# Optimization experiments

Measured on AMD Instinct MI355X. Metric: run time of the kernel, lower is better.

## Reference

```python
import jax, jax.numpy as jnp
import numpy as np

D_MODEL = 1024
H = 16
D_FF = 2048
EPS = 1e-5


def _ln(x, g, b):
    m = jnp.mean(x, axis=-1, keepdims=True)
    v = jnp.mean((x - m) ** 2, axis=-1, keepdims=True)
    return (x - m) * jax.lax.rsqrt(v + EPS) * g + b


def setup_inputs() -> dict:
    key = jax.random.key(0)
    ks = jax.random.split(key, 16)
    d, dff = D_MODEL, D_FF
    s = 1.0 / np.sqrt(d)
    inp = {
        "x": jax.random.normal(ks[0], (2, 2048, d), jnp.float32),
        "Wq": jax.random.normal(ks[1], (d, d), jnp.float32) * s,
        "bq": jax.random.normal(ks[2], (d,), jnp.float32) * 0.01,
        "Wk": jax.random.normal(ks[3], (d, d), jnp.float32) * s,
        "bk": jax.random.normal(ks[4], (d,), jnp.float32) * 0.01,
        "Wv": jax.random.normal(ks[5], (d, d), jnp.float32) * s,
        "bv": jax.random.normal(ks[6], (d,), jnp.float32) * 0.01,
        "Wo": jax.random.normal(ks[7], (d, d), jnp.float32) * s,
        "bo": jax.random.normal(ks[8], (d,), jnp.float32) * 0.01,
        "ln1_g": 1.0 + 0.1 * jax.random.normal(ks[9], (d,), jnp.float32),
        "ln1_b": 0.01 * jax.random.normal(ks[10], (d,), jnp.float32),
        "ln2_g": 1.0 + 0.1 * jax.random.normal(ks[11], (d,), jnp.float32),
        "ln2_b": 0.01 * jax.random.normal(ks[12], (d,), jnp.float32),
        "W1": jax.random.normal(ks[13], (d, dff), jnp.float32) * s,
        "b1": 0.01 * jax.random.normal(ks[14], (dff,), jnp.float32),
        "W2": jax.random.normal(ks[15], (dff, d), jnp.float32) * (1.0 / np.sqrt(dff)),
        "b2": jnp.zeros((d,), jnp.float32),
    }
    return inp


def reference(x, Wq, bq, Wk, bk, Wv, bv, Wo, bo, ln1_g, ln1_b, ln2_g, ln2_b, W1, b1, W2, b2):
    b, s, d = x.shape
    dk = d // H

    # --- sublayer 1: pre-LN self-attention with residual (dropout = eval/identity) ---
    y = _ln(x, ln1_g, ln1_b)
    q = (y @ Wq + bq).reshape(b, s, H, dk).transpose(0, 2, 1, 3)  # (b,h,s,dk)
    k = (y @ Wk + bk).reshape(b, s, H, dk).transpose(0, 2, 1, 3)
    v = (y @ Wv + bv).reshape(b, s, H, dk).transpose(0, 2, 1, 3)
    scores = jnp.einsum("bhqd,bhkd->bhqk", q, k) / jnp.sqrt(jnp.float32(dk))
    attn = jax.nn.softmax(scores, axis=-1)
    o = jnp.einsum("bhqk,bhkd->bhqd", attn, v)  # (b,h,s,dk)
    # faithful to original bug: transpose last two dims then flat reshape
    o = jnp.swapaxes(o, -1, -2).reshape(b, s, d)  # (b,h,dk,s) -> (b,s,d)
    x = x + (o @ Wo + bo)

    # --- sublayer 2: pre-LN FFN with residual ---
    y2 = _ln(x, ln2_g, ln2_b)
    f = jax.nn.relu(y2 @ W1 + b1) @ W2 + b2
    return x + f
```

## Files before the change

### kernel.cpp

```cpp
#include <hip/hip_runtime.h>
#include <hip/hip_bf16.h>

#define D_MODEL 1024
#define NHEAD 16
#define DK 64
#define DFF 2048
#define SEQ 2048
#define NBATCH 2
#define NTOK (NBATCH*SEQ)

typedef __attribute__((ext_vector_type(8))) short bf16x8;
typedef __attribute__((ext_vector_type(4))) float f32x4;
typedef __attribute__((ext_vector_type(16))) float f32x16;
typedef __attribute__((ext_vector_type(4))) short s16x4;

#if __has_builtin(__builtin_amdgcn_exp2f)
#define EXP2(x) __builtin_amdgcn_exp2f(x)
#else
#define EXP2(x) exp2f(x)
#endif

__device__ __forceinline__ short f2bf(float f) {
    union { float f; unsigned u; } v; v.f = f;
    unsigned r = v.u + 0x7FFFu + ((v.u >> 16) & 1u);
    return (short)(r >> 16);
}

__device__ __forceinline__ void gld16(void* lds, const void* g) {
    __builtin_amdgcn_global_load_lds(
        (const __attribute__((address_space(1))) void*)g,
        (__attribute__((address_space(3))) void*)lds, 16, 0, 0);
}

struct TP6 { const float* src[6]; short* dst[6]; int K[6], N[6], nx[6]; };
__global__ __launch_bounds__(256) void k_prolog(TP6 tp, const float* __restrict__ x,
                                                const float* __restrict__ g,
                                                const float* __restrict__ bta,
                                                short* __restrict__ y)
{
    __shared__ float t[32][33];
    int id = blockIdx.x;
    if (id >= 8192) {
        int row = (id - 8192) * 4 + (threadIdx.x >> 6);
        int lane = threadIdx.x & 63;
        const float* xr = x + (size_t)row * D_MODEL;
        float4 v[4];
        float s = 0.f, s2 = 0.f;
#pragma unroll
        for (int c = 0; c < 4; ++c) {
            v[c] = *(const float4*)(xr + c * 256 + lane * 4);
            s  += v[c].x + v[c].y + v[c].z + v[c].w;
            s2 += v[c].x * v[c].x + v[c].y * v[c].y + v[c].z * v[c].z + v[c].w * v[c].w;
        }
#pragma unroll
        for (int off = 1; off < 64; off <<= 1) {
            s  += __shfl_xor(s, off, 64);
            s2 += __shfl_xor(s2, off, 64);
        }
        float mean = s * (1.f / 1024.f);
        float var  = s2 * (1.f / 1024.f) - mean * mean;
        float rs = rsqrtf(var + 1e-5f);
        short* yr = y + (size_t)row * D_MODEL;
#pragma unroll
        for (int c = 0; c < 4; ++c) {
            int idx = c * 256 + lane * 4;
            float4 gg = *(const float4*)(g + idx);
            float4 bb = *(const float4*)(bta + idx);
            s16x4 o;
            o.x = f2bf((v[c].x - mean) * rs * gg.x + bb.x);
            o.y = f2bf((v[c].y - mean) * rs * gg.y + bb.y);
            o.z = f2bf((v[c].z - mean) * rs * gg.z + bb.z);
            o.w = f2bf((v[c].w - mean) * rs * gg.w + bb.w);
            *(s16x4*)(yr + idx) = o;
        }
        return;
    }
    int seg, tt;
    if (id < 4096)      { seg = id >> 10; tt = id & 1023; }
    else if (id < 6144) { seg = 4; tt = id - 4096; }
    else                { seg = 5; tt = id - 6144; }
    const float* W = tp.src[seg];
    short* WT = tp.dst[seg];
    int K = tp.K[seg], N = tp.N[seg], nx = tp.nx[seg];
    int bx = tt % nx, by = tt / nx;
    int tid = threadIdx.x;
    int n0 = bx * 32, k0 = by * 32;
#pragma unroll
    for (int p = 0; p < 4; ++p) {
        int idx = p * 256 + tid, r = idx >> 5, c = idx & 31;
        t[r][c] = W[(size_t)(k0 + r) * N + (n0 + c)];
    }
    __syncthreads();
#pragma unroll
    for (int p = 0; p < 4; ++p) {
        int idx = p * 256 + tid, r = idx >> 5, c = idx & 31;
        WT[(size_t)(n0 + r) * K + (k0 + c)] = f2bf(t[c][r]);
    }
}

__global__ __launch_bounds__(256) void k_layernorm(const float* __restrict__ x,
                                                   const float* __restrict__ g,
                                                   const float* __restrict__ bta,
                                                   short* __restrict__ y)
{
    int row = blockIdx.x * 4 + (threadIdx.x >> 6);
    int lane = threadIdx.x & 63;
    const float* xr = x + (size_t)row * D_MODEL;
    float4 v[4];
    float s = 0.f, s2 = 0.f;
#pragma unroll
    for (int c = 0; c < 4; ++c) {
        v[c] = *(const float4*)(xr + c * 256 + lane * 4);
        s  += v[c].x + v[c].y + v[c].z + v[c].w;
        s2 += v[c].x * v[c].x + v[c].y * v[c].y + v[c].z * v[c].z + v[c].w * v[c].w;
    }
#pragma unroll
    for (int off = 1; off < 64; off <<= 1) {
        s  += __shfl_xor(s, off, 64);
        s2 += __shfl_xor(s2, off, 64);
    }
    float mean = s * (1.f / 1024.f);
    float var  = s2 * (1.f / 1024.f) - mean * mean;
    float rs = rsqrtf(var + 1e-5f);
    short* yr = y + (size_t)row * D_MODEL;
#pragma unroll
    for (int c = 0; c < 4; ++c) {
        int idx = c * 256 + lane * 4;
        float4 gg = *(const float4*)(g + idx);
        float4 bb = *(const float4*)(bta + idx);
        s16x4 o;
        o.x = f2bf((v[c].x - mean) * rs * gg.x + bb.x);
        o.y = f2bf((v[c].y - mean) * rs * gg.y + bb.y);
        o.z = f2bf((v[c].z - mean) * rs * gg.z + bb.z);
        o.w = f2bf((v[c].w - mean) * rs * gg.w + bb.w);
        *(s16x4*)(yr + idx) = o;
    }
}

template<int EPI, int BN, int THREADS>
__global__ __launch_bounds__(THREADS, (THREADS == 512) ? 8 : 4) void k_gemm(
    const short* __restrict__ A, const short* __restrict__ BT, int N, int K,
    const float* __restrict__ bias, const float* __restrict__ bias2, const float* __restrict__ bias3,
    const float* __restrict__ resid, float* __restrict__ outF,
    short* __restrict__ outB, short* __restrict__ outQ, short* __restrict__ outK, short* __restrict__ outV)
{
    constexpr int CW = (THREADS == 512) ? 4 : 2;
    __shared__ __align__(16) short sA[3][128 * 32];
    __shared__ __align__(16) short sB[3][BN * 32];
    int tid = threadIdx.x;
    int lane = tid & 63, wid = tid >> 6;
    int wr = wid / CW, wc = wid % CW;
    int l31 = lane & 31, hi = lane >> 5;

    int gx = gridDim.x;
    int nwg = gx * gridDim.y;
    int orig = blockIdx.x + blockIdx.y * gx;
    int wg = (orig & 7) * (nwg >> 3) + (orig >> 3);
    int bx = wg % gx, by = wg / gx;

    const short* Ab = A + (size_t)by * 128 * K;
    const short* Bb = BT + (size_t)bx * BN * K;

    auto src = [&](const short* base, int cc) {
        int r = cc >> 2, s = cc & 3;
        return (const char*)(base + (size_t)r * K) + ((s ^ ((r >> 1) & 3)) << 4);
    };
    const char *pA0 = src(Ab, tid), *pA1 = nullptr, *pB0;
    if constexpr (THREADS == 512) {
        pB0 = src(Bb, tid);
    } else {
        pA1 = src(Ab, 256 + tid);
        pB0 = src(Bb, tid & (BN * 4 - 1));
    }

    auto stage = [&](int buf) {
        if constexpr (THREADS == 512) {
            gld16(&sA[buf][tid * 8], pA0);  pA0 += 64;
            gld16(&sB[buf][tid * 8], pB0);  pB0 += 64;
        } else {
            gld16(&sA[buf][tid * 8], pA0);          pA0 += 64;
            gld16(&sA[buf][(256 + tid) * 8], pA1);  pA1 += 64;
            gld16(&sB[buf][(tid & (BN * 4 - 1)) * 8], pB0);  pB0 += 64;
        }
    };

    f32x16 acc0 = {0,0,0,0,0,0,0,0,0,0,0,0,0,0,0,0};
    f32x16 acc1 = {0,0,0,0,0,0,0,0,0,0,0,0,0,0,0,0};

    const int NT = K / 32;
    stage(0);
    stage(1);
    int cur = 0;
    for (int t = 0; t < NT; ++t) {
        if (t + 2 < NT) {
            int nb3 = cur + 2; if (nb3 >= 3) nb3 -= 3;
            stage(nb3);
            if constexpr (THREADS == 512) asm volatile("s_waitcnt vmcnt(4)" ::: "memory");
            else                          asm volatile("s_waitcnt vmcnt(6)" ::: "memory");
        } else if (t + 1 < NT) {
            if constexpr (THREADS == 512) asm volatile("s_waitcnt vmcnt(2)" ::: "memory");
            else                          asm volatile("s_waitcnt vmcnt(3)" ::: "memory");
        } else {
            asm volatile("s_waitcnt vmcnt(0)" ::: "memory");
        }
        __builtin_amdgcn_s_barrier();
        int rb = wc * 32 + l31;
        int swb = (rb >> 1) & 3;
        bf16x8 b0 = *(const bf16x8*)((const char*)sB[cur] + rb * 64 + ((hi ^ swb) << 4));
        bf16x8 b1 = *(const bf16x8*)((const char*)sB[cur] + rb * 64 + (((2 + hi) ^ swb) << 4));
        {
            int ra = wr * 64 + l31;
            int swa = (ra >> 1) & 3;
            bf16x8 a0 = *(const bf16x8*)((const char*)sA[cur] + ra * 64 + ((hi ^ swa) << 4));
            acc0 = __builtin_amdgcn_mfma_f32_32x32x16_bf16(a0, b0, acc0, 0, 0, 0);
            bf16x8 a1 = *(const bf16x8*)((const char*)sA[cur] + ra * 64 + (((2 + hi) ^ swa) << 4));
            acc0 = __builtin_amdgcn_mfma_f32_32x32x16_bf16(a1, b1, acc0, 0, 0, 0);
        }
        {
            int ra = wr * 64 + 32 + l31;
            int swa = (ra >> 1) & 3;
            bf16x8 a0 = *(const bf16x8*)((const char*)sA[cur] + ra * 64 + ((hi ^ swa) << 4));
            acc1 = __builtin_amdgcn_mfma_f32_32x32x16_bf16(a0, b0, acc1, 0, 0, 0);
            bf16x8 a1 = *(const bf16x8*)((const char*)sA[cur] + ra * 64 + (((2 + hi) ^ swa) << 4));
            acc1 = __builtin_amdgcn_mfma_f32_32x32x16_bf16(a1, b1, acc1, 0, 0, 0);
        }
        __builtin_amdgcn_s_barrier();
        ++cur; if (cur >= 3) cur = 0;
    }

    int n = bx * BN + wc * 32 + l31;
    int mb = by * 128 + wr * 64 + 4 * hi;
    if constexpr (EPI == 0) {
        int seg = n >> 10, nn = n & 1023;
        int h = nn >> 6, dd = nn & 63;
        int bb = (by * 128) >> 11;
        if (seg == 0) {
            float bs = bias[nn];
            short* p = outQ + (size_t)(bb * NHEAD + h) * SEQ * DK + dd;
#pragma unroll
            for (int i = 0; i < 2; ++i)
#pragma unroll
                for (int reg = 0; reg < 16; ++reg) {
                    int ss = (mb + i * 32 + (reg & 3) + 8 * (reg >> 2)) & 2047;
                    float v = (i == 0) ? acc0[reg] : acc1[reg];
                    p[(size_t)ss * DK] = f2bf((v + bs) * 0.18033688011112042f);
                }
        } else if (seg == 1) {
            float bs = bias2[nn];
            short* p = outK + (size_t)(bb * NHEAD + h) * SEQ * DK + dd;
#pragma unroll
            for (int i = 0; i < 2; ++i)
#pragma unroll
                for (int reg = 0; reg < 16; ++reg) {
                    int ss = (mb + i * 32 + (reg & 3) + 8 * (reg >> 2)) & 2047;
                    float v = (i == 0) ? acc0[reg] : acc1[reg];
                    p[(size_t)ss * DK] = f2bf(v + bs);
                }
        } else {
            float bs = bias3[nn];
            short* p = outV + ((size_t)(bb * NHEAD + h) * DK + dd) * SEQ;
#pragma unroll
            for (int i = 0; i < 2; ++i)
#pragma unroll
                for (int reg = 0; reg < 16; ++reg) {
                    int ss = (mb + i * 32 + (reg & 3) + 8 * (reg >> 2)) & 2047;
                    float v = (i == 0) ? acc0[reg] : acc1[reg];
                    p[ss] = f2bf(v + bs);
                }
        }
    } else if constexpr (EPI == 1 || EPI == 3) {
        float bs = bias[n];
#pragma unroll
        for (int i = 0; i < 2; ++i)
#pragma unroll
            for (int reg = 0; reg < 16; ++reg) {
                int m = mb + i * 32 + (reg & 3) + 8 * (reg >> 2);
                float v = (i == 0) ? acc0[reg] : acc1[reg];
                size_t idx = (size_t)m * N + n;
                outF[idx] = v + bs + resid[idx];
            }
    } else {
        float bs = bias[n];
#pragma unroll
        for (int i = 0; i < 2; ++i)
#pragma unroll
            for (int reg = 0; reg < 16; ++reg) {
                int m = mb + i * 32 + (reg & 3) + 8 * (reg >> 2);
                float v = (i == 0) ? acc0[reg] : acc1[reg];
                float r2 = v + bs;
                outB[(size_t)m * N + n] = f2bf(r2 > 0.f ? r2 : 0.f);
            }
    }
}

__global__ __launch_bounds__(256) void k_attn(const short* __restrict__ Q, const short* __restrict__ Kk,
                                              const short* __restrict__ Vt, short* __restrict__ Operm)
{
    __shared__ __align__(16) short sMem[2][2][64 * 64];
    int tid = threadIdx.x, lane = tid & 63;
    int wid = tid >> 6;
    int qg = wid >> 1, ks = wid & 1;
    int l31 = lane & 31, hi = lane >> 5;

    int orig = blockIdx.x + blockIdx.y * 32;
    int lg = (orig & 7) * 128 + (orig >> 3);
    int bh = lg >> 5, qt = lg & 31;
    int b = bh >> 4, h = bh & 15;
    int q0 = qt * 64 + qg * 32;
    const short* Qp = Q + (size_t)bh * SEQ * DK;
    const short* Kp = Kk + (size_t)bh * SEQ * DK;
    const short* Vp = Vt + (size_t)bh * DK * SEQ;

    bf16x8 qf[4];
#pragma unroll
    for (int kb = 0; kb < 4; ++kb)
        qf[kb] = *(const bf16x8*)(Qp + (size_t)(q0 + l31) * DK + kb * 16 + hi * 8);

    int c0 = tid, c1 = 256 + tid;
    int r0 = c0 >> 3, r1 = c1 >> 3;
    const char* pK0 = (const char*)(Kp + (size_t)r0 * DK) + (((c0 & 7) ^ (r0 & 7)) << 4);
    const char* pK1 = (const char*)(Kp + (size_t)r1 * DK) + (((c1 & 7) ^ (r1 & 7)) << 4);
    const char* pV0 = (const char*)(Vp + (size_t)r0 * SEQ) + (((c0 & 7) ^ (r0 & 7)) << 4);
    const char* pV1 = (const char*)(Vp + (size_t)r1 * SEQ) + (((c1 & 7) ^ (r1 & 7)) << 4);

    auto stage = [&](int buf) {
        gld16(&sMem[buf][0][c0 * 8], pK0);  pK0 += 8192;
        gld16(&sMem[buf][0][c1 * 8], pK1);  pK1 += 8192;
        gld16(&sMem[buf][1][c0 * 8], pV0);  pV0 += 128;
        gld16(&sMem[buf][1][c1 * 8], pV1);  pV1 += 128;
    };

    f32x16 Oa0 = {0,0,0,0,0,0,0,0,0,0,0,0,0,0,0,0};
    f32x16 Oa1 = {0,0,0,0,0,0,0,0,0,0,0,0,0,0,0,0};
    float lsum = 0.f;

    stage(0);
    const int NT = SEQ / 64;
    int krow = ks * 32 + l31;
    int sw = (l31 & 7) << 4;
    for (int t = 0; t < NT; ++t) {
        int cur = t & 1;
        if (t + 1 < NT) {
            stage(cur ^ 1);
            asm volatile("s_waitcnt vmcnt(4)" ::: "memory");
        } else {
            asm volatile("s_waitcnt vmcnt(0)" ::: "memory");
        }
        __builtin_amdgcn_s_barrier();
        const char* sKc = (const char*)sMem[cur][0];
        const char* sVc = (const char*)sMem[cur][1];

        f32x16 sc = {0,0,0,0,0,0,0,0,0,0,0,0,0,0,0,0};
        __builtin_amdgcn_s_setprio(1);
#pragma unroll
        for (int kb = 0; kb < 4; ++kb) {
            int cb = (kb * 32 + hi * 16) ^ sw;
            bf16x8 kf = *(const bf16x8*)(sKc + krow * 128 + cb);
            sc = __builtin_amdgcn_mfma_f32_32x32x16_bf16(kf, qf[kb], sc, 0, 0, 0);
        }
        __builtin_amdgcn_s_setprio(0);

        unsigned W[4][2];
#pragma unroll
        for (int tt = 0; tt < 4; ++tt) {
            float pa_ = EXP2(sc[4*tt+0]), pb_ = EXP2(sc[4*tt+1]);
            float pc_ = EXP2(sc[4*tt+2]), pd_ = EXP2(sc[4*tt+3]);
            lsum += (pa_ + pb_) + (pc_ + pd_);
            asm("v_cvt_pk_bf16_f32 %0, %1, %2" : "=v"(W[tt][0]) : "v"(pa_), "v"(pb_));
            asm("v_cvt_pk_bf16_f32 %0, %1, %2" : "=v"(W[tt][1]) : "v"(pc_), "v"(pd_));
        }

        auto pv_step = [&](unsigned a0, unsigned a1, unsigned b0v, unsigned b1v, int kslice) {
            asm("v_permlane32_swap_b32 %0, %1" : "+v"(a0), "+v"(b0v));
            asm("v_permlane32_swap_b32 %0, %1" : "+v"(a1), "+v"(b1v));
            union { unsigned u[4]; bf16x8 v; } pa;
            pa.u[0] = a0; pa.u[1] = a1; pa.u[2] = b0v; pa.u[3] = b1v;
            int cb = (kslice * 32 + hi * 16) ^ sw;
            bf16x8 vf0 = *(const bf16x8*)(sVc + l31 * 128 + cb);
            bf16x8 vf1 = *(const bf16x8*)(sVc + (32 + l31) * 128 + cb);
            Oa0 = __builtin_amdgcn_mfma_f32_32x32x16_bf16(pa.v, vf0, Oa0, 0, 0, 0);
            Oa1 = __builtin_amdgcn_mfma_f32_32x32x16_bf16(pa.v, vf1, Oa1, 0, 0, 0);
        };
        __builtin_amdgcn_s_setprio(1);
        pv_step(W[0][0], W[0][1], W[1][0], W[1][1], ks * 2 + 0);
        pv_step(W[2][0], W[2][1], W[3][0], W[3][1], ks * 2 + 1);
        __builtin_amdgcn_s_setprio(0);
        __builtin_amdgcn_s_barrier();
    }

    lsum += __shfl_xor(lsum, 32, 64);

    float* mrg = (float*)sMem;
    if (ks == 1) {
        float* m0 = mrg + (qg * 64 + lane) * 33;
#pragma unroll
        for (int i = 0; i < 16; ++i) m0[i] = Oa0[i];
#pragma unroll
        for (int i = 0; i < 16; ++i) m0[16 + i] = Oa1[i];
        m0[32] = lsum;
    }
    __syncthreads();
    if (ks == 0) {
        const float* m0 = mrg + (qg * 64 + lane) * 33;
#pragma unroll
        for (int i = 0; i < 16; ++i) Oa0[i] += m0[i];
#pragma unroll
        for (int i = 0; i < 16; ++i) Oa1[i] += m0[16 + i];
        lsum += m0[32];

        float rlv[16];
#pragma unroll
        for (int tt = 0; tt < 4; ++tt)
#pragma unroll
            for (int rr = 0; rr < 4; ++rr) {
                float ts = __shfl(lsum, 4 * hi + 8 * tt + rr, 64);
                rlv[4 * tt + rr] = 1.f / ts;
            }

        int qcol = (q0 & 1023) + 4 * hi;
        int qhi = q0 >> 10;
#pragma unroll
        for (int db = 0; db < 2; ++db) {
            const f32x16& O = db ? Oa1 : Oa0;
            int dd = db * 32 + l31;
            size_t rowoff = ((size_t)b * SEQ + h * 128 + 2 * dd + qhi) * D_MODEL + qcol;
#pragma unroll
            for (int tt = 0; tt < 4; ++tt) {
                s16x4 o;
                o.x = f2bf(O[4*tt+0] * rlv[4*tt+0]);
                o.y = f2bf(O[4*tt+1] * rlv[4*tt+1]);
                o.z = f2bf(O[4*tt+2] * rlv[4*tt+2]);
                o.w = f2bf(O[4*tt+3] * rlv[4*tt+3]);
                *(s16x4*)(Operm + rowoff + 8 * tt) = o;
            }
        }
    }
}

extern "C" void kernel_launch(void* const* d_in, const int* in_sizes, int n_in,
                              void* d_out, int out_size, void* d_ws, size_t ws_size,
                              hipStream_t stream)
{
    const float* x   = (const float*)d_in[0];
    const float* Wq  = (const float*)d_in[1];
    const float* bq  = (const float*)d_in[2];
    const float* Wk  = (const float*)d_in[3];
    const float* bk  = (const float*)d_in[4];
    const float* Wv  = (const float*)d_in[5];
    const float* bv  = (const float*)d_in[6];
    const float* Wo  = (const float*)d_in[7];
    const float* bo  = (const float*)d_in[8];
    const float* g1  = (const float*)d_in[9];
    const float* b1l = (const float*)d_in[10];
    const float* g2  = (const float*)d_in[11];
    const float* b2l = (const float*)d_in[12];
    const float* W1  = (const float*)d_in[13];
    const float* b1  = (const float*)d_in[14];
    const float* W2  = (const float*)d_in[15];
    const float* b2  = (const float*)d_in[16];
    float* out = (float*)d_out;

    char* ws = (char*)d_ws;
    size_t off = 0;
    auto alloc = [&](size_t bytes) {
        char* p = ws + off;
        off += (bytes + 255) & ~(size_t)255;
        return p;
    };
    short* WqkvT = (short*)alloc((size_t)3072 * 1024 * 2);
    short* WoT   = (short*)alloc((size_t)1024 * 1024 * 2);
    short* W1T   = (short*)alloc((size_t)2048 * 1024 * 2);
    short* W2T   = (short*)alloc((size_t)1024 * 2048 * 2);
    short* Y     = (short*)alloc((size_t)NTOK * 1024 * 2);
    short* Qb    = (short*)alloc((size_t)NTOK * 1024 * 2);
    short* Kb    = (short*)alloc((size_t)NTOK * 1024 * 2);
    short* Vtb   = (short*)alloc((size_t)NTOK * 1024 * 2);
    short* Operm = (short*)alloc((size_t)NTOK * 1024 * 2);
    float* X1    = (float*)alloc((size_t)NTOK * 1024 * 4);
    short* F1    = (short*)alloc((size_t)NTOK * 2048 * 2);

    TP6 tp;
    tp.src[0] = Wq; tp.dst[0] = WqkvT;                tp.K[0] = 1024; tp.N[0] = 1024; tp.nx[0] = 32;
    tp.src[1] = Wk; tp.dst[1] = WqkvT + 1024 * 1024;  tp.K[1] = 1024; tp.N[1] = 1024; tp.nx[1] = 32;
    tp.src[2] = Wv; tp.dst[2] = WqkvT + 2048 * 1024;  tp.K[2] = 1024; tp.N[2] = 1024; tp.nx[2] = 32;
    tp.src[3] = Wo; tp.dst[3] = WoT;                  tp.K[3] = 1024; tp.N[3] = 1024; tp.nx[3] = 32;
    tp.src[4] = W1; tp.dst[4] = W1T;                  tp.K[4] = 1024; tp.N[4] = 2048; tp.nx[4] = 64;
    tp.src[5] = W2; tp.dst[5] = W2T;                  tp.K[5] = 2048; tp.N[5] = 1024; tp.nx[5] = 32;
    k_prolog<<<8192 + 1024, 256, 0, stream>>>(tp, x, g1, b1l, Y);

    k_gemm<0,128,512><<<dim3(24, 32), 512, 0, stream>>>(Y, WqkvT, 3072, 1024,
        bq, bk, bv, nullptr, nullptr, nullptr, Qb, Kb, Vtb);

    k_attn<<<dim3(32, 32), 256, 0, stream>>>(Qb, Kb, Vtb, Operm);

    k_gemm<1,64,256><<<dim3(16, 32), 256, 0, stream>>>(Operm, WoT, 1024, 1024,
        bo, nullptr, nullptr, x, X1, nullptr, nullptr, nullptr, nullptr);

    k_layernorm<<<NTOK / 4, 256, 0, stream>>>(X1, g2, b2l, Y);

    k_gemm<2,128,512><<<dim3(16, 32), 512, 0, stream>>>(Y, W1T, 2048, 1024,
        b1, nullptr, nullptr, nullptr, nullptr, F1, nullptr, nullptr, nullptr);

    k_gemm<3,64,256><<<dim3(16, 32), 256, 0, stream>>>(F1, W2T, 1024, 2048,
        b2, nullptr, nullptr, X1, out, nullptr, nullptr, nullptr, nullptr);
}
```

Baseline: 195.2 us.

## Use 256x128 block tiles with 2x2 MFMA per wave for QKV and FFN1 GEMMs

Adds a new GEMM kernel for the QKV projection and the first FFN layer. It uses 256x128 tiles with 8 waves, each computing a 64x64 sub-tile through a 2x2 grid of 32x32 MFMAs, and drops from triple to double LDS buffering. This gives more reuse of each loaded fragment and fewer global loads per FLOP. In exchange the grid is halved, so fewer workgroups fill the CUs, registers per wave go up, and there is less prefetch depth to hide latency.

```diff
diff --git a/kernel.cpp b/kernel.cpp
--- a/kernel.cpp
+++ b/kernel.cpp
@@ -137,19 +137,17 @@
     }
 }
 
-template<int EPI, int BN, int THREADS>
-__global__ __launch_bounds__(THREADS, (THREADS == 512) ? 8 : 4) void k_gemm(
+template<int EPI>
+__global__ __launch_bounds__(512, 4) void k_gemm_big(
     const short* __restrict__ A, const short* __restrict__ BT, int N, int K,
     const float* __restrict__ bias, const float* __restrict__ bias2, const float* __restrict__ bias3,
-    const float* __restrict__ resid, float* __restrict__ outF,
     short* __restrict__ outB, short* __restrict__ outQ, short* __restrict__ outK, short* __restrict__ outV)
 {
-    constexpr int CW = (THREADS == 512) ? 4 : 2;
-    __shared__ __align__(16) short sA[3][128 * 32];
-    __shared__ __align__(16) short sB[3][BN * 32];
+    __shared__ __align__(16) short sA[2][256 * 32];
+    __shared__ __align__(16) short sB[2][128 * 32];
     int tid = threadIdx.x;
     int lane = tid & 63, wid = tid >> 6;
-    int wr = wid / CW, wc = wid % CW;
+    int wr = wid >> 1, wc = wid & 1;
     int l31 = lane & 31, hi = lane >> 5;
 
     int gx = gridDim.x;
@@ -158,30 +156,152 @@
     int wg = (orig & 7) * (nwg >> 3) + (orig >> 3);
     int bx = wg % gx, by = wg / gx;
 
-    const short* Ab = A + (size_t)by * 128 * K;
-    const short* Bb = BT + (size_t)bx * BN * K;
+    const short* Ab = A + (size_t)by * 256 * K;
+    const short* Bb = BT + (size_t)bx * 128 * K;
 
     auto src = [&](const short* base, int cc) {
         int r = cc >> 2, s = cc & 3;
         return (const char*)(base + (size_t)r * K) + ((s ^ ((r >> 1) & 3)) << 4);
     };
-    const char *pA0 = src(Ab, tid), *pA1 = nullptr, *pB0;
-    if constexpr (THREADS == 512) {
-        pB0 = src(Bb, tid);
+    const char* pA0 = src(Ab, tid);
+    const char* pA1 = src(Ab, 512 + tid);
+    const char* pB0 = src(Bb, tid);
+
+    auto stage = [&](int buf) {
+        gld16(&sA[buf][tid * 8], pA0);          pA0 += 64;
+        gld16(&sA[buf][(512 + tid) * 8], pA1);  pA1 += 64;
+        gld16(&sB[buf][tid * 8], pB0);          pB0 += 64;
+    };
+
+    f32x16 acc[2][2];
+#pragma unroll
+    for (int i = 0; i < 2; ++i)
+#pragma unroll
+        for (int j = 0; j < 2; ++j)
+            acc[i][j] = (f32x16){0,0,0,0,0,0,0,0,0,0,0,0,0,0,0,0};
+
+    const int NT = K / 32;
+    stage(0);
+    for (int t = 0; t < NT; ++t) {
+        int cur = t & 1;
+        if (t + 1 < NT) {
+            stage(cur ^ 1);
+            asm volatile("s_waitcnt vmcnt(3)" ::: "memory");
+        } else {
+            asm volatile("s_waitcnt vmcnt(0)" ::: "memory");
+        }
+        __builtin_amdgcn_s_barrier();
+        const char* sAc = (const char*)sA[cur];
+        const char* sBc = (const char*)sB[cur];
+#pragma unroll
+        for (int ksub = 0; ksub < 2; ++ksub) {
+            int sl = ksub * 2 + hi;
+            int rb0 = wc * 64 + l31, rb1 = rb0 + 32;
+            bf16x8 b0 = *(const bf16x8*)(sBc + rb0 * 64 + ((sl ^ ((rb0 >> 1) & 3)) << 4));
+            bf16x8 b1 = *(const bf16x8*)(sBc + rb1 * 64 + ((sl ^ ((rb1 >> 1) & 3)) << 4));
+            int ra0 = wr * 64 + l31, ra1 = ra0 + 32;
+            bf16x8 a0 = *(const bf16x8*)(sAc + ra0 * 64 + ((sl ^ ((ra0 >> 1) & 3)) << 4));
+            bf16x8 a1 = *(const bf16x8*)(sAc + ra1 * 64 + ((sl ^ ((ra1 >> 1) & 3)) << 4));
+            acc[0][0] = __builtin_amdgcn_mfma_f32_32x32x16_bf16(a0, b0, acc[0][0], 0, 0, 0);
+            acc[0][1] = __builtin_amdgcn_mfma_f32_32x32x16_bf16(a0, b1, acc[0][1], 0, 0, 0);
+            acc[1][0] = __builtin_amdgcn_mfma_f32_32x32x16_bf16(a1, b0, acc[1][0], 0, 0, 0);
+            acc[1][1] = __builtin_amdgcn_mfma_f32_32x32x16_bf16(a1, b1, acc[1][1], 0, 0, 0);
+        }
+        __builtin_amdgcn_s_barrier();
+    }
+
+    int nb = bx * 128 + wc * 64 + l31;
+    int mb = by * 256 + wr * 64 + 4 * hi;
+    if constexpr (EPI == 0) {
+        int seg = nb >> 10;
+        int bb = (by * 256) >> 11;
+#pragma unroll
+        for (int j = 0; j < 2; ++j) {
+            int nn = (nb + j * 32) & 1023;
+            int h = nn >> 6, dd = nn & 63;
+            if (seg == 0) {
+                float bs = bias[nn];
+                short* p = outQ + (size_t)(bb * NHEAD + h) * SEQ * DK + dd;
+#pragma unroll
+                for (int i = 0; i < 2; ++i)
+#pragma unroll
+                    for (int reg = 0; reg < 16; ++reg) {
+                        int ss = (mb + i * 32 + (reg & 3) + 8 * (reg >> 2)) & 2047;
+                        p[(size_t)ss * DK] = f2bf((acc[i][j][reg] + bs) * 0.18033688011112042f);
+                    }
+            } else if (seg == 1) {
+                float bs = bias2[nn];
+                short* p = outK + (size_t)(bb * NHEAD + h) * SEQ * DK + dd;
+#pragma unroll
+                for (int i = 0; i < 2; ++i)
+#pragma unroll
+                    for (int reg = 0; reg < 16; ++reg) {
+                        int ss = (mb + i * 32 + (reg & 3) + 8 * (reg >> 2)) & 2047;
+                        p[(size_t)ss * DK] = f2bf(acc[i][j][reg] + bs);
+                    }
+            } else {
+                float bs = bias3[nn];
+                short* p = outV + ((size_t)(bb * NHEAD + h) * DK + dd) * SEQ;
+#pragma unroll
+                for (int i = 0; i < 2; ++i)
+#pragma unroll
+                    for (int reg = 0; reg < 16; ++reg) {
+                        int ss = (mb + i * 32 + (reg & 3) + 8 * (reg >> 2)) & 2047;
+                        p[ss] = f2bf(acc[i][j][reg] + bs);
+                    }
+            }
+        }
     } else {
-        pA1 = src(Ab, 256 + tid);
-        pB0 = src(Bb, tid & (BN * 4 - 1));
-    }
+#pragma unroll
+        for (int j = 0; j < 2; ++j) {
+            int n = nb + j * 32;
+            float bs = bias[n];
+#pragma unroll
+            for (int i = 0; i < 2; ++i)
+#pragma unroll
+                for (int reg = 0; reg < 16; ++reg) {
+                    int m = mb + i * 32 + (reg & 3) + 8 * (reg >> 2);
+                    float r2 = acc[i][j][reg] + bs;
+                    outB[(size_t)m * N + n] = f2bf(r2 > 0.f ? r2 : 0.f);
+                }
+        }
+    }
+}
+
+template<int EPI>
+__global__ __launch_bounds__(256, 4) void k_gemm(
+    const short* __restrict__ A, const short* __restrict__ BT, int N, int K,
+    const float* __restrict__ bias, const float* __restrict__ resid, float* __restrict__ outF)
+{
+    constexpr int BN = 64;
+    __shared__ __align__(16) short sA[3][128 * 32];
+    __shared__ __align__(16) short sB[3][BN * 32];
+    int tid = threadIdx.x;
+    int lane = tid & 63, wid = tid >> 6;
+    int wr = wid >> 1, wc = wid & 1;
+    int l31 = lane & 31, hi = lane >> 5;
+
+    int gx = gridDim.x;
+    int nwg = gx * gridDim.y;
+    int orig = blockIdx.x + blockIdx.y * gx;
+    int wg = (orig & 7) * (nwg >> 3) + (orig >> 3);
+    int bx = wg % gx, by = wg / gx;
+
+    const short* Ab = A + (size_t)by * 128 * K;
+    const short* Bb = BT + (size_t)bx * BN * K;
+
+    auto src = [&](const short* base, int cc) {
+        int r = cc >> 2, s = cc & 3;
+        return (const char*)(base + (size_t)r * K) + ((s ^ ((r >> 1) & 3)) << 4);
+    };
+    const char* pA0 = src(Ab, tid);
+    const char* pA1 = src(Ab, 256 + tid);
+    const char* pB0 = src(Bb, tid & (BN * 4 - 1));
 
     auto stage = [&](int buf) {
-        if constexpr (THREADS == 512) {
-            gld16(&sA[buf][tid * 8], pA0);  pA0 += 64;
-            gld16(&sB[buf][tid * 8], pB0);  pB0 += 64;
-        } else {
-            gld16(&sA[buf][tid * 8], pA0);          pA0 += 64;
-            gld16(&sA[buf][(256 + tid) * 8], pA1);  pA1 += 64;
-            gld16(&sB[buf][(tid & (BN * 4 - 1)) * 8], pB0);  pB0 += 64;
-        }
+        gld16(&sA[buf][tid * 8], pA0);          pA0 += 64;
+        gld16(&sA[buf][(256 + tid) * 8], pA1);  pA1 += 64;
+        gld16(&sB[buf][(tid & (BN * 4 - 1)) * 8], pB0);  pB0 += 64;
     };
 
     f32x16 acc0 = {0,0,0,0,0,0,0,0,0,0,0,0,0,0,0,0};
@@ -195,11 +315,9 @@
         if (t + 2 < NT) {
             int nb3 = cur + 2; if (nb3 >= 3) nb3 -= 3;
             stage(nb3);
-            if constexpr (THREADS == 512) asm volatile("s_waitcnt vmcnt(4)" ::: "memory");
-            else                          asm volatile("s_waitcnt vmcnt(6)" ::: "memory");
+            asm volatile("s_waitcnt vmcnt(6)" ::: "memory");
         } else if (t + 1 < NT) {
-            if constexpr (THREADS == 512) asm volatile("s_waitcnt vmcnt(2)" ::: "memory");
-            else                          asm volatile("s_waitcnt vmcnt(3)" ::: "memory");
+            asm volatile("s_waitcnt vmcnt(3)" ::: "memory");
         } else {
             asm volatile("s_waitcnt vmcnt(0)" ::: "memory");
         }
@@ -230,67 +348,16 @@
 
     int n = bx * BN + wc * 32 + l31;
     int mb = by * 128 + wr * 64 + 4 * hi;
-    if constexpr (EPI == 0) {
-        int seg = n >> 10, nn = n & 1023;
-        int h = nn >> 6, dd = nn & 63;
-        int bb = (by * 128) >> 11;
-        if (seg == 0) {
-            float bs = bias[nn];
-            short* p = outQ + (size_t)(bb * NHEAD + h) * SEQ * DK + dd;
-#pragma unroll
-            for (int i = 0; i < 2; ++i)
-#pragma unroll
-                for (int reg = 0; reg < 16; ++reg) {
-                    int ss = (mb + i * 32 + (reg & 3) + 8 * (reg >> 2)) & 2047;
-                    float v = (i == 0) ? acc0[reg] : acc1[reg];
-                    p[(size_t)ss * DK] = f2bf((v + bs) * 0.18033688011112042f);
-                }
-        } else if (seg == 1) {
-            float bs = bias2[nn];
-            short* p = outK + (size_t)(bb * NHEAD + h) * SEQ * DK + dd;
-#pragma unroll
-            for (int i = 0; i < 2; ++i)
-#pragma unroll
-                for (int reg = 0; reg < 16; ++reg) {
-                    int ss = (mb + i * 32 + (reg & 3) + 8 * (reg >> 2)) & 2047;
-                    float v = (i == 0) ? acc0[reg] : acc1[reg];
-                    p[(size_t)ss * DK] = f2bf(v + bs);
-                }
-        } else {
-            float bs = bias3[nn];
-            short* p = outV + ((size_t)(bb * NHEAD + h) * DK + dd) * SEQ;
-#pragma unroll
-            for (int i = 0; i < 2; ++i)
-#pragma unroll
-                for (int reg = 0; reg < 16; ++reg) {
-                    int ss = (mb + i * 32 + (reg & 3) + 8 * (reg >> 2)) & 2047;
-                    float v = (i == 0) ? acc0[reg] : acc1[reg];
-                    p[ss] = f2bf(v + bs);
-                }
-        }
-    } else if constexpr (EPI == 1 || EPI == 3) {
-        float bs = bias[n];
-#pragma unroll
-        for (int i = 0; i < 2; ++i)
-#pragma unroll
-            for (int reg = 0; reg < 16; ++reg) {
-                int m = mb + i * 32 + (reg & 3) + 8 * (reg >> 2);
-                float v = (i == 0) ? acc0[reg] : acc1[reg];
-                size_t idx = (size_t)m * N + n;
-                outF[idx] = v + bs + resid[idx];
-            }
-    } else {
-        float bs = bias[n];
-#pragma unroll
-        for (int i = 0; i < 2; ++i)
-#pragma unroll
-            for (int reg = 0; reg < 16; ++reg) {
-                int m = mb + i * 32 + (reg & 3) + 8 * (reg >> 2);
-                float v = (i == 0) ? acc0[reg] : acc1[reg];
-                float r2 = v + bs;
-                outB[(size_t)m * N + n] = f2bf(r2 > 0.f ? r2 : 0.f);
-            }
-    }
+    float bs = bias[n];
+#pragma unroll
+    for (int i = 0; i < 2; ++i)
+#pragma unroll
+        for (int reg = 0; reg < 16; ++reg) {
+            int m = mb + i * 32 + (reg & 3) + 8 * (reg >> 2);
+            float v = (i == 0) ? acc0[reg] : acc1[reg];
+            size_t idx = (size_t)m * N + n;
+            outF[idx] = v + bs + resid[idx];
+        }
 }
 
 __global__ __launch_bounds__(256) void k_attn(const short* __restrict__ Q, const short* __restrict__ Kk,
@@ -488,19 +555,17 @@
     tp.src[5] = W2; tp.dst[5] = W2T;                  tp.K[5] = 2048; tp.N[5] = 1024; tp.nx[5] = 32;
     k_prolog<<<8192 + 1024, 256, 0, stream>>>(tp, x, g1, b1l, Y);
 
-    k_gemm<0,128,512><<<dim3(24, 32), 512, 0, stream>>>(Y, WqkvT, 3072, 1024,
-        bq, bk, bv, nullptr, nullptr, nullptr, Qb, Kb, Vtb);
+    k_gemm_big<0><<<dim3(24, 16), 512, 0, stream>>>(Y, WqkvT, 3072, 1024,
+        bq, bk, bv, nullptr, Qb, Kb, Vtb);
 
     k_attn<<<dim3(32, 32), 256, 0, stream>>>(Qb, Kb, Vtb, Operm);
 
-    k_gemm<1,64,256><<<dim3(16, 32), 256, 0, stream>>>(Operm, WoT, 1024, 1024,
-        bo, nullptr, nullptr, x, X1, nullptr, nullptr, nullptr, nullptr);
+    k_gemm<1><<<dim3(16, 32), 256, 0, stream>>>(Operm, WoT, 1024, 1024, bo, x, X1);
 
     k_layernorm<<<NTOK / 4, 256, 0, stream>>>(X1, g2, b2l, Y);
 
-    k_gemm<2,128,512><<<dim3(16, 32), 512, 0, stream>>>(Y, W1T, 2048, 1024,
-        b1, nullptr, nullptr, nullptr, nullptr, F1, nullptr, nullptr, nullptr);
-
-    k_gemm<3,64,256><<<dim3(16, 32), 256, 0, stream>>>(F1, W2T, 1024, 2048,
-        b2, nullptr, nullptr, X1, out, nullptr, nullptr, nullptr, nullptr);
-}
+    k_gemm_big<2><<<dim3(16, 16), 512, 0, stream>>>(Y, W1T, 2048, 1024,
+        b1, nullptr, nullptr, F1, nullptr, nullptr, nullptr);
+
+    k_gemm<3><<<dim3(16, 32), 256, 0, stream>>>(F1, W2T, 1024, 2048, b2, X1, out);
+}
```

Measured after the change: 199.5 us. 1.02x slower.
